# Performance work log

Measured on AMD Instinct MI355X. Metric: run time of the kernel, lower is better.

Reference implementation:

```python
import math
import jax, jax.numpy as jnp
import numpy as np

HIDDEN = 1024
HEADS = 16
HEAD_DIM = HIDDEN // HEADS
PRIME = 7
MAX_ITERS = 10
ENT_THRESH = 0.2
PRIME_SCALE = 1.0 / math.sqrt(PRIME * HEAD_DIM)
EPS = 1e-6


def setup_inputs() -> dict:
    key = jax.random.key(0)
    ks = jax.random.split(key, 6)
    B, S = 2, 2048
    w = 0.02
    return {
        "hidden_states": jax.random.normal(ks[0], (B, S, HIDDEN), jnp.float32),
        "q_w": jax.random.normal(ks[1], (HIDDEN, HIDDEN), jnp.float32) * w,
        "q_b": jnp.zeros((HIDDEN,), jnp.float32),
        "k_w": jax.random.normal(ks[2], (HIDDEN, HIDDEN), jnp.float32) * w,
        "k_b": jnp.zeros((HIDDEN,), jnp.float32),
        "v_w": jax.random.normal(ks[3], (HIDDEN, HIDDEN), jnp.float32) * w,
        "v_b": jnp.zeros((HIDDEN,), jnp.float32),
        "o_w": jax.random.normal(ks[4], (HIDDEN, HIDDEN), jnp.float32) * w,
        "o_b": jnp.zeros((HIDDEN,), jnp.float32),
        "attention_mask": jnp.ones((B, S), jnp.int32),
    }


def _split_heads(x):
    B, S, _ = x.shape
    return x.reshape(B, S, HEADS, HEAD_DIM).transpose(0, 2, 1, 3)


def reference(hidden_states, q_w, q_b, k_w, k_b, v_w, v_b, o_w, o_b, attention_mask):
    B, S, _ = hidden_states.shape
    # projections (torch Linear: x @ W^T + b)
    q = _split_heads(hidden_states @ q_w.T + q_b) * PRIME_SCALE  # [B,H,S,hd]
    k = _split_heads(hidden_states @ k_w.T + k_b)
    v = _split_heads(hidden_states @ v_w.T + v_b)

    scores = jnp.einsum("bhqd,bhkd->bhqk", q, k)  # [B,H,S,S]
    mask = attention_mask[:, None, None, :]
    scores = jnp.where(mask == 0, -jnp.inf, scores)
    attn = jax.nn.softmax(scores, axis=-1)  # dropout p=0 (eval)

    base = jnp.einsum("bhqk,bhkd->bhqd", attn, v)  # attention_weights @ v

    # entropy of the (fixed) attention weights: [B,H]
    entropy = -jnp.sum(attn * jnp.log(attn + EPS), axis=-1).mean(axis=-1)
    avg_entropy = entropy.mean()

    # loop never changes attn, so entropy is constant: either break at i=1 or run all
    full = base
    for i in range(1, MAX_ITERS):
        blend = 1.0 / (1.0 + math.exp(-i / MAX_ITERS))          # sigmoid(i/max)
        res_scale = 0.5 + 0.5 * blend                            # resonance scale
        full = (1.0 - blend) * full + blend * (res_scale * base)

    out_heads = jnp.where(avg_entropy < ENT_THRESH, base, full)  # [B,H,S,hd]

    merged = out_heads.transpose(0, 2, 1, 3).reshape(B, S, HIDDEN)
    return merged @ o_w.T + o_b
```

## Files before the change

### kernel.cpp

```cpp
#include <hip/hip_runtime.h>
#include <hip/hip_bf16.h>
#include <stdint.h>


#define PRIME_SCALE 0.047245559126654356f
#define LOG2E       1.4426950408889634f
#define LN2         0.6931471805599453f
#define QSCALE      (PRIME_SCALE * LOG2E)
#define BLEND_C     0.85096556f

#if __has_builtin(__builtin_amdgcn_exp2f)
#define EXP2(x) __builtin_amdgcn_exp2f(x)
#else
#define EXP2(x) exp2f(x)
#endif

typedef __attribute__((ext_vector_type(8))) short short8;
typedef __attribute__((ext_vector_type(4))) float f32x4;

__device__ __forceinline__ unsigned short f2bf(float x) {
    union { float f; unsigned int u; } v; v.f = x;
    unsigned int r = (v.u + 0x7fffu + ((v.u >> 16) & 1u)) >> 16;
    return (unsigned short)r;
}
__device__ __forceinline__ unsigned short f2bf_fast(float x) {
    union { float f; unsigned int u; } v; v.f = x;
    return (unsigned short)((v.u + 0x8000u) >> 16);
}
__device__ __forceinline__ float bf2f(unsigned short x) {
    union { unsigned int u; float f; } v; v.u = ((unsigned int)x) << 16;
    return v.f;
}
__device__ __forceinline__ unsigned cvtpk_bf16(float lo, float hi) {
    unsigned r;
    asm("v_cvt_pk_bf16_f32 %0, %1, %2" : "=v"(r) : "v"(lo), "v"(hi));
    return r;
}

__device__ __forceinline__ void glds16(const unsigned short* g, unsigned short* l) {
    __builtin_amdgcn_global_load_lds((const __attribute__((address_space(1))) unsigned int*)g,
                                     (__attribute__((address_space(3))) unsigned int*)l,
                                     16, 0, 0);
}

__global__ void zero_out_f32(float* p, int n) {
    int i = blockIdx.x * 256 + threadIdx.x;
    if (i < n) p[i] = 0.f;
}

__global__ __launch_bounds__(256) void cvt5(
    const float* __restrict__ s0, const float* __restrict__ s1, const float* __restrict__ s2,
    const float* __restrict__ s3, const float* __restrict__ s4,
    unsigned short* __restrict__ d0, unsigned short* __restrict__ d1, unsigned short* __restrict__ d2,
    unsigned short* __restrict__ d3, unsigned short* __restrict__ d4, float* entp)
{
    if (blockIdx.x == 0 && threadIdx.x == 0) entp[0] = 0.f;
    unsigned int i = blockIdx.x * 256 + threadIdx.x;
    const float* s; unsigned short* d; unsigned int off;
    if (i < (1u << 20)) { s = s0; d = d0; off = i; }
    else {
        unsigned int j = i - (1u << 20);
        unsigned int sel = j >> 18; off = j & 0x3FFFFu;
        s = sel == 0 ? s1 : sel == 1 ? s2 : sel == 2 ? s3 : s4;
        d = sel == 0 ? d1 : sel == 1 ? d2 : sel == 2 ? d3 : d4;
    }
    float4 v = ((const float4*)s)[off];
    ushort4 p; p.x = f2bf(v.x); p.y = f2bf(v.y); p.z = f2bf(v.z); p.w = f2bf(v.w);
    ((ushort4*)d)[off] = p;
}

__global__ __launch_bounds__(256) void gemm_qkv(
    const unsigned short* __restrict__ hsb,
    const unsigned short* __restrict__ qwb, const unsigned short* __restrict__ kwb,
    const unsigned short* __restrict__ vwb,
    const float* __restrict__ qb, const float* __restrict__ kb, const float* __restrict__ vb,
    unsigned short* __restrict__ Qo, unsigned short* __restrict__ Ko, unsigned short* __restrict__ Vto)
{
    const int bid = blockIdx.x;
    const int op = bid >> 8, local = bid & 255;
    const unsigned short *A, *B; const float* bias; unsigned short* C;
    int m0, n0, ldc, biasRow; float scale;
    if (op == 0)      { A = hsb; B = qwb; bias = qb; C = Qo;  m0 = (local >> 3) * 128; n0 = (local & 7) * 128;  ldc = 1024; biasRow = 0; scale = QSCALE; }
    else if (op == 1) { A = hsb; B = kwb; bias = kb; C = Ko;  m0 = (local >> 3) * 128; n0 = (local & 7) * 128;  ldc = 1024; biasRow = 0; scale = 1.f; }
    else              { A = vwb; B = hsb; bias = vb; C = Vto; m0 = (local >> 5) * 128; n0 = (local & 31) * 128; ldc = 4096; biasRow = 1; scale = 1.f; }

    __shared__ unsigned short As[128 * 32];
    __shared__ unsigned short Bs[128 * 32];
    const int t = threadIdx.x, lane = t & 63, w = t >> 6;
    const int quad = lane >> 4, l15 = lane & 15;
    const int wr = (w >> 1) * 64, wc = (w & 1) * 64;
    const int srow = lane >> 2, scol = (lane & 3) * 8;

    f32x4 acc[4][4];
#pragma unroll
    for (int i = 0; i < 4; ++i)
#pragma unroll
        for (int j = 0; j < 4; ++j) acc[i][j] = (f32x4){0.f, 0.f, 0.f, 0.f};

    for (int kk = 0; kk < 32; ++kk) {
        const int k0 = kk * 32;
#pragma unroll
        for (int j = 0; j < 2; ++j) {
            int row = (w * 2 + j) * 16 + srow;
            glds16(&A[(size_t)(m0 + row) * 1024 + k0 + scol], &As[(w * 2 + j) * 512]);
            glds16(&B[(size_t)(n0 + row) * 1024 + k0 + scol], &Bs[(w * 2 + j) * 512]);
        }
        __syncthreads();
        short8 af[4], bf[4];
#pragma unroll
        for (int mt = 0; mt < 4; ++mt) af[mt] = *(const short8*)&As[(wr + mt * 16 + l15) * 32 + quad * 8];
#pragma unroll
        for (int nt = 0; nt < 4; ++nt) bf[nt] = *(const short8*)&Bs[(wc + nt * 16 + l15) * 32 + quad * 8];
#pragma unroll
        for (int mt = 0; mt < 4; ++mt)
#pragma unroll
            for (int nt = 0; nt < 4; ++nt)
                acc[mt][nt] = __builtin_amdgcn_mfma_f32_16x16x32_bf16(af[mt], bf[nt], acc[mt][nt], 0, 0, 0);
        __syncthreads();
    }
#pragma unroll
    for (int mt = 0; mt < 4; ++mt) {
#pragma unroll
        for (int nt = 0; nt < 4; ++nt) {
            int n = n0 + wc + nt * 16 + l15;
#pragma unroll
            for (int r = 0; r < 4; ++r) {
                int m = m0 + wr + mt * 16 + quad * 4 + r;
                float bval = biasRow ? bias[m] : bias[n];
                C[(size_t)m * ldc + n] = f2bf((acc[mt][nt][r] + bval) * scale);
            }
        }
    }
}


#define QK_SOFTMAX(MASKED)                                                          \
    _Pragma("unroll")                                                               \
    for (int nt = 0; nt < 4; ++nt) {                                                \
        int krow = nt * 16 + l15;                                                   \
        short8 kf0 = *(const short8*)&Ks[cur][krow * 64 + ((quad ^ (krow & 7)) * 8)];       \
        short8 kf1 = *(const short8*)&Ks[cur][krow * 64 + (((quad + 4) ^ (krow & 7)) * 8)]; \
        f32x4 sv[4];                                                                \
        __builtin_amdgcn_s_setprio(1);                                              \
        _Pragma("unroll")                                                           \
        for (int st = 0; st < 4; ++st) {                                            \
            sv[st] = __builtin_amdgcn_mfma_f32_16x16x32_bf16(kf0, qa[st][0], (f32x4){0.f, 0.f, 0.f, 0.f}, 0, 0, 0); \
            sv[st] = __builtin_amdgcn_mfma_f32_16x16x32_bf16(kf1, qa[st][1], sv[st], 0, 0, 0); \
        }                                                                           \
        __builtin_amdgcn_s_setprio(0);                                              \
        unsigned mb = 0xFu;                                                         \
        if (MASKED) {                                                               \
            unsigned mw = (nt & 2) ? mwB : mwA;                                     \
            mb = (mw >> (((nt & 1) << 4) + (quad << 2))) & 0xFu;                    \
        }                                                                           \
        _Pragma("unroll")                                                           \
        for (int st = 0; st < 4; ++st) {                                            \
            float s0 = sv[st][0], s1 = sv[st][1], s2 = sv[st][2], s3 = sv[st][3];   \
            if (MASKED) {                                                           \
                s0 = (mb & 1u) ? s0 : -1.0e30f;                                     \
                s1 = (mb & 2u) ? s1 : -1.0e30f;                                     \
                s2 = (mb & 4u) ? s2 : -1.0e30f;                                     \
                s3 = (mb & 8u) ? s3 : -1.0e30f;                                     \
            }                                                                       \
            float p0 = EXP2(s0), p1 = EXP2(s1), p2 = EXP2(s2), p3 = EXP2(s3);       \
            l_r[st] += (p0 + p1) + (p2 + p3);                                       \
            T_r[st] += (p0 * s0 + p1 * s1) + (p2 * s2 + p3 * s3);                   \
            pk[nt][st][0] = cvtpk_bf16(p0, p1);                                     \
            pk[nt][st][1] = cvtpk_bf16(p2, p3);                                     \
        }                                                                           \
    }

__global__ __launch_bounds__(256, 2) void flash_split(
    const unsigned short* __restrict__ Q,
    const unsigned short* __restrict__ K,
    const unsigned short* __restrict__ Vt,
    const int* __restrict__ mask,
    unsigned short* __restrict__ O0, unsigned short* __restrict__ O1,
    float* __restrict__ lpart, float* __restrict__ Tpart)
{
    const int qt = blockIdx.x;
    const int bh = blockIdx.y;
    const int z  = blockIdx.z;
    const int b = bh >> 4, h = bh & 15;
    const int t = threadIdx.x, lane = t & 63, w = t >> 6;
    const int quad = lane >> 4, l15 = lane & 15;
    const int r8 = lane >> 3, ch8 = lane & 7;
    const int kt0 = z * 16, kt1 = kt0 + 16;
    unsigned short* __restrict__ Opart = z ? O1 : O0;

    __shared__ unsigned short Qs[256 * 64];
    __shared__ unsigned short Ks[2][64 * 64];
    __shared__ unsigned short Vs[2][64 * 64];

    const int* maskb = mask + b * 2048;

    {
        const int row0 = w * 16;
#pragma unroll
        for (int i = 0; i < 2; ++i) {
            int row = row0 + i * 8 + r8;
            int c = ch8 ^ (row & 7);
            glds16(&K[(size_t)(b * 2048 + kt0 * 64 + row) * 1024 + h * 64 + c * 8], &Ks[0][(row0 + i * 8) * 64]);
            glds16(&Vt[(size_t)(h * 64 + row) * 4096 + b * 2048 + kt0 * 64 + c * 8], &Vs[0][(row0 + i * 8) * 64]);
        }
    }
#pragma unroll
    for (int i = 0; i < 8; ++i) {
        int f = i * 256 + t; int row = f >> 3, c = f & 7;
        uint4 v = *(const uint4*)&Q[(size_t)(b * 2048 + qt * 256 + row) * 1024 + h * 64 + c * 8];
        int rx = row & 15;
        uint2 plo; plo.x = v.x; plo.y = v.y;
        uint2 phi; phi.x = v.z; phi.y = v.w;
        *(uint2*)&Qs[row * 64 + (((2 * c) ^ rx) << 2)]     = plo;
        *(uint2*)&Qs[row * 64 + (((2 * c + 1) ^ rx) << 2)] = phi;
    }
    __syncthreads();

    short8 qa[4][2];
#pragma unroll
    for (int st = 0; st < 4; ++st) {
        int prow = (w * 64 + st * 16 + l15) * 64;
#pragma unroll
        for (int hf = 0; hf < 2; ++hf) {
            int p0 = hf * 8 + quad * 2;
            union { uint2 u2[2]; short8 s8; } uu;
            uu.u2[0] = *(const uint2*)&Qs[prow + ((p0 ^ l15) << 2)];
            uu.u2[1] = *(const uint2*)&Qs[prow + (((p0 + 1) ^ l15) << 2)];
            qa[st][hf] = uu.s8;
        }
    }

    float l_r[4] = {0.f, 0.f, 0.f, 0.f}, T_r[4] = {0.f, 0.f, 0.f, 0.f};
    f32x4 o_acc[4][4];
#pragma unroll
    for (int st = 0; st < 4; ++st)
#pragma unroll
        for (int nt = 0; nt < 4; ++nt) o_acc[st][nt] = (f32x4){0.f, 0.f, 0.f, 0.f};

    int mv = maskb[kt0 * 64 + lane];

    for (int kt = kt0; kt < kt1; ++kt) {
        const int cur = kt & 1;
        int mv_next = 0;
        if (kt < kt1 - 1) {
            const int kn = (kt + 1) * 64;
            const int row0 = w * 16;
#pragma unroll
            for (int i = 0; i < 2; ++i) {
                int row = row0 + i * 8 + r8;
                int c = ch8 ^ (row & 7);
                glds16(&K[(size_t)(b * 2048 + kn + row) * 1024 + h * 64 + c * 8], &Ks[cur ^ 1][(row0 + i * 8) * 64]);
                glds16(&Vt[(size_t)(h * 64 + row) * 4096 + b * 2048 + kn + c * 8], &Vs[cur ^ 1][(row0 + i * 8) * 64]);
            }
            mv_next = maskb[kn + lane];
        }
        unsigned long long bal = __ballot(mv != 0);
        unsigned mwA = (unsigned)bal, mwB = (unsigned)(bal >> 32);

        unsigned pk[4][4][2];
        if ((mwA & mwB) == 0xFFFFFFFFu) {
            QK_SOFTMAX(0)
        } else {
            QK_SOFTMAX(1)
        }

#pragma unroll
        for (int ks = 0; ks < 2; ++ks) {
            short8 pa[4];
#pragma unroll
            for (int st = 0; st < 4; ++st) {
                unsigned a0 = pk[2 * ks][st][0], a1 = pk[2 * ks][st][1];
                unsigned b0 = pk[2 * ks + 1][st][0], b1 = pk[2 * ks + 1][st][1];
                asm("v_permlane32_swap_b32 %0, %1" : "+v"(a0), "+v"(b0));
                asm("v_permlane32_swap_b32 %0, %1" : "+v"(a1), "+v"(b1));
                asm("v_permlane16_swap_b32 %0, %1" : "+v"(a0), "+v"(b0));
                asm("v_permlane16_swap_b32 %0, %1" : "+v"(a1), "+v"(b1));
                union { unsigned u[4]; short8 s8; } uu;
                uu.u[0] = a0; uu.u[1] = a1; uu.u[2] = b0; uu.u[3] = b1;
                pa[st] = uu.s8;
            }
            __builtin_amdgcn_s_setprio(1);
#pragma unroll
            for (int nt = 0; nt < 4; ++nt) {
                int vrow = nt * 16 + l15;
                short8 vf = *(const short8*)&Vs[cur][vrow * 64 + ((((ks * 4 + quad)) ^ (vrow & 7)) * 8)];
#pragma unroll
                for (int st = 0; st < 4; ++st)
                    o_acc[st][nt] = __builtin_amdgcn_mfma_f32_16x16x32_bf16(pa[st], vf, o_acc[st][nt], 0, 0, 0);
            }
            __builtin_amdgcn_s_setprio(0);
        }
        __syncthreads();
        mv = mv_next;
    }

#pragma unroll
    for (int st = 0; st < 4; ++st) {
        float l = l_r[st], T = T_r[st];
        l += __shfl_xor(l, 16); T += __shfl_xor(T, 16);
        l += __shfl_xor(l, 32); T += __shfl_xor(T, 32);
        if (lane < 16) {
            int qrow = qt * 256 + w * 64 + st * 16 + l15;
            int li = z * 65536 + bh * 2048 + qrow;
            lpart[li] = l; Tpart[li] = T;
        }
#pragma unroll
        for (int r = 0; r < 4; ++r) {
            int mrow = b * 2048 + qt * 256 + w * 64 + st * 16 + quad * 4 + r;
#pragma unroll
            for (int nt = 0; nt < 4; ++nt)
                Opart[(size_t)mrow * 1024 + h * 64 + nt * 16 + l15] = f2bf_fast(o_acc[st][nt][r]);
        }
    }
}

__global__ __launch_bounds__(256) void combine_split(
    unsigned short* __restrict__ O0, const unsigned short* __restrict__ O1,
    const float* __restrict__ lpart)
{
    unsigned idx = blockIdx.x * 256 + threadIdx.x;
    int mrow = idx >> 8;
    int c4 = (idx & 255) << 2;
    int h = c4 >> 6;
    int b = mrow >> 11, qrow = mrow & 2047;
    int li = (b * 16 + h) * 2048 + qrow;
    float l = lpart[li] + lpart[65536 + li];
    float inv = 1.0f / l;

    ushort4 a = ((const ushort4*)O0)[idx];
    ushort4 c = ((const ushort4*)O1)[idx];
    ushort4 o;
    o.x = f2bf_fast((bf2f(a.x) + bf2f(c.x)) * inv);
    o.y = f2bf_fast((bf2f(a.y) + bf2f(c.y)) * inv);
    o.z = f2bf_fast((bf2f(a.z) + bf2f(c.z)) * inv);
    o.w = f2bf_fast((bf2f(a.w) + bf2f(c.w)) * inv);
    ((ushort4*)O0)[idx] = o;
}

__global__ __launch_bounds__(256) void entropy_k(
    const float* __restrict__ lpart, const float* __restrict__ Tpart,
    float* __restrict__ entp)
{
    __shared__ float wsum[4];
    int idx = blockIdx.x * 256 + threadIdx.x;
    float acc = 0.f;
#pragma unroll
    for (int i = 0; i < 4; ++i) {
        int r = idx * 4 + i;
        float l = lpart[r] + lpart[65536 + r];
        float T = Tpart[r] + Tpart[65536 + r];
        acc += __log2f(l) - T / l;
    }
    acc += __shfl_xor(acc, 1);
    acc += __shfl_xor(acc, 2);
    acc += __shfl_xor(acc, 4);
    acc += __shfl_xor(acc, 8);
    acc += __shfl_xor(acc, 16);
    acc += __shfl_xor(acc, 32);
    int lane = threadIdx.x & 63, w = threadIdx.x >> 6;
    if (lane == 0) wsum[w] = acc;
    __syncthreads();
    if (threadIdx.x == 0)
        atomicAdd(entp, LN2 * (wsum[0] + wsum[1] + wsum[2] + wsum[3]));
}

__global__ __launch_bounds__(256) void gemm_out_bf(
    const unsigned short* __restrict__ A, const unsigned short* __restrict__ Bw,
    const float* __restrict__ bias, const float* __restrict__ entp,
    float* __restrict__ C)
{
    const float avg = entp[0] * (1.0f / 65536.0f);
    const float scale = (avg < 0.2f) ? 1.0f : BLEND_C;

    const int m0 = blockIdx.x * 128;
    const int n0 = blockIdx.y * 64;
    __shared__ unsigned short As[128 * 32];
    __shared__ unsigned short Bs[64 * 32];
    const int t = threadIdx.x, lane = t & 63, w = t >> 6;
    const int quad = lane >> 4, l15 = lane & 15;
    const int wr = (w >> 1) * 64, wc = (w & 1) * 32;
    const int srow = lane >> 2, scol = (lane & 3) * 8;

    f32x4 acc[4][2];
#pragma unroll
    for (int i = 0; i < 4; ++i)
#pragma unroll
        for (int j = 0; j < 2; ++j) acc[i][j] = (f32x4){0.f, 0.f, 0.f, 0.f};

    for (int kk = 0; kk < 32; ++kk) {
        const int k0 = kk * 32;
#pragma unroll
        for (int j = 0; j < 2; ++j) {
            int row = (w * 2 + j) * 16 + srow;
            glds16(&A[(size_t)(m0 + row) * 1024 + k0 + scol], &As[(w * 2 + j) * 512]);
        }
        {
            int row = w * 16 + srow;
            glds16(&Bw[(size_t)(n0 + row) * 1024 + k0 + scol], &Bs[w * 512]);
        }
        __syncthreads();
        short8 af[4], bf[2];
#pragma unroll
        for (int mt = 0; mt < 4; ++mt) af[mt] = *(const short8*)&As[(wr + mt * 16 + l15) * 32 + quad * 8];
#pragma unroll
        for (int nt = 0; nt < 2; ++nt) bf[nt] = *(const short8*)&Bs[(wc + nt * 16 + l15) * 32 + quad * 8];
#pragma unroll
        for (int mt = 0; mt < 4; ++mt)
#pragma unroll
            for (int nt = 0; nt < 2; ++nt)
                acc[mt][nt] = __builtin_amdgcn_mfma_f32_16x16x32_bf16(af[mt], bf[nt], acc[mt][nt], 0, 0, 0);
        __syncthreads();
    }
#pragma unroll
    for (int mt = 0; mt < 4; ++mt) {
#pragma unroll
        for (int nt = 0; nt < 2; ++nt) {
            int n = n0 + wc + nt * 16 + l15;
#pragma unroll
            for (int r = 0; r < 4; ++r) {
                int m = m0 + wr + mt * 16 + quad * 4 + r;
                C[(size_t)m * 1024 + n] = scale * acc[mt][nt][r] + bias[n];
            }
        }
    }
}

extern "C" void kernel_launch(void* const* d_in, const int* in_sizes, int n_in,
                              void* d_out, int out_size, void* d_ws, size_t ws_size,
                              hipStream_t stream)
{
    const float* hs = (const float*)d_in[0];
    const float* qw = (const float*)d_in[1];
    const float* qb = (const float*)d_in[2];
    const float* kw = (const float*)d_in[3];
    const float* kb = (const float*)d_in[4];
    const float* vw = (const float*)d_in[5];
    const float* vb = (const float*)d_in[6];
    const float* ow = (const float*)d_in[7];
    const float* ob = (const float*)d_in[8];
    const int*   mask = (const int*)d_in[9];
    float* out = (float*)d_out;

    const size_t MB = 1024 * 1024;
    char* ws = (char*)d_ws;
    dim3 blk(256);

    if (ws_size >= 50 * MB) {
        unsigned short* hsb = (unsigned short*)(ws);
        unsigned short* Q   = (unsigned short*)(ws + 8 * MB);
        unsigned short* Kp  = (unsigned short*)(ws + 16 * MB);
        unsigned short* Vt  = (unsigned short*)(ws + 24 * MB);
        unsigned short* qwb = (unsigned short*)(ws + 32 * MB);
        unsigned short* kwb = (unsigned short*)(ws + 34 * MB);
        unsigned short* vwb = (unsigned short*)(ws + 36 * MB);
        unsigned short* owb = (unsigned short*)(ws + 38 * MB);
        float* entp         = (float*)(ws + 40 * MB);
        unsigned short* Op1 = (unsigned short*)(ws + 41 * MB);
        float* lpart        = (float*)(ws + 49 * MB);
        float* Tpart        = (float*)(ws + 49 * MB + 524288);
        unsigned short* Op0 = hsb;

        cvt5<<<dim3(8192), blk, 0, stream>>>(hs, qw, kw, vw, ow, hsb, qwb, kwb, vwb, owb, entp);
        gemm_qkv<<<dim3(768), blk, 0, stream>>>(hsb, qwb, kwb, vwb, qb, kb, vb, Q, Kp, Vt);
        flash_split<<<dim3(8, 32, 2), blk, 0, stream>>>(Q, Kp, Vt, mask, Op0, Op1, lpart, Tpart);
        combine_split<<<dim3(4096), blk, 0, stream>>>(Op0, Op1, lpart);
        entropy_k<<<dim3(64), blk, 0, stream>>>(lpart, Tpart, entp);
        gemm_out_bf<<<dim3(32, 16), blk, 0, stream>>>(Op0, owb, ob, entp, out);
    } else {
        zero_out_f32<<<dim3((out_size + 255) / 256), blk, 0, stream>>>(out, out_size);
    }
}
```

Measured before the change: 205.1 us.

## Split each flash K tile across two warp groups with in-LDS output reduction

The flash attention kernel now runs 512 threads per block. Two groups of four warps each process half of every 64-key tile, and their partial O accumulators and l/T sums are reduced through shared memory at the end. Q fragments are loaded straight from global memory into registers, which removes the Q staging buffer in LDS and cuts shared memory per block so more blocks can be resident. The cost is a cross-warp reduction epilogue with extra barriers, plus duplicated Q loads and K/V tile traffic shared by more waves.

```diff
diff --git a/kernel.cpp b/kernel.cpp
--- a/kernel.cpp
+++ b/kernel.cpp
@@ -136,10 +136,10 @@
 
 #define QK_SOFTMAX(MASKED)                                                          \
     _Pragma("unroll")                                                               \
-    for (int nt = 0; nt < 4; ++nt) {                                                \
-        int krow = nt * 16 + l15;                                                   \
-        short8 kf0 = *(const short8*)&Ks[cur][krow * 64 + ((quad ^ (krow & 7)) * 8)];       \
-        short8 kf1 = *(const short8*)&Ks[cur][krow * 64 + (((quad + 4) ^ (krow & 7)) * 8)]; \
+    for (int nt2 = 0; nt2 < 2; ++nt2) {                                             \
+        int krow = wk * 32 + nt2 * 16 + l15;                                        \
+        short8 kf0 = *(const short8*)&Ks[cur * 4096 + krow * 64 + ((quad ^ (krow & 7)) * 8)];       \
+        short8 kf1 = *(const short8*)&Ks[cur * 4096 + krow * 64 + (((quad + 4) ^ (krow & 7)) * 8)]; \
         f32x4 sv[4];                                                                \
         __builtin_amdgcn_s_setprio(1);                                              \
         _Pragma("unroll")                                                           \
@@ -149,10 +149,7 @@
         }                                                                           \
         __builtin_amdgcn_s_setprio(0);                                              \
         unsigned mb = 0xFu;                                                         \
-        if (MASKED) {                                                               \
-            unsigned mw = (nt & 2) ? mwB : mwA;                                     \
-            mb = (mw >> (((nt & 1) << 4) + (quad << 2))) & 0xFu;                    \
-        }                                                                           \
+        if (MASKED) mb = (mw >> ((nt2 << 4) + (quad << 2))) & 0xFu;                 \
         _Pragma("unroll")                                                           \
         for (int st = 0; st < 4; ++st) {                                            \
             float s0 = sv[st][0], s1 = sv[st][1], s2 = sv[st][2], s3 = sv[st][3];   \
@@ -165,12 +162,12 @@
             float p0 = EXP2(s0), p1 = EXP2(s1), p2 = EXP2(s2), p3 = EXP2(s3);       \
             l_r[st] += (p0 + p1) + (p2 + p3);                                       \
             T_r[st] += (p0 * s0 + p1 * s1) + (p2 * s2 + p3 * s3);                   \
-            pk[nt][st][0] = cvtpk_bf16(p0, p1);                                     \
-            pk[nt][st][1] = cvtpk_bf16(p2, p3);                                     \
+            pk[nt2][st][0] = cvtpk_bf16(p0, p1);                                    \
+            pk[nt2][st][1] = cvtpk_bf16(p2, p3);                                    \
         }                                                                           \
     }
 
-__global__ __launch_bounds__(256, 2) void flash_split(
+__global__ __launch_bounds__(512, 4) void flash_split(
     const unsigned short* __restrict__ Q,
     const unsigned short* __restrict__ K,
     const unsigned short* __restrict__ Vt,
@@ -183,51 +180,33 @@
     const int z  = blockIdx.z;
     const int b = bh >> 4, h = bh & 15;
     const int t = threadIdx.x, lane = t & 63, w = t >> 6;
+    const int wq = w & 3, wk = w >> 2;
     const int quad = lane >> 4, l15 = lane & 15;
     const int r8 = lane >> 3, ch8 = lane & 7;
     const int kt0 = z * 16, kt1 = kt0 + 16;
     unsigned short* __restrict__ Opart = z ? O1 : O0;
 
-    __shared__ unsigned short Qs[256 * 64];
-    __shared__ unsigned short Ks[2][64 * 64];
-    __shared__ unsigned short Vs[2][64 * 64];
+    __shared__ __align__(16) unsigned short smem[16384];
+    unsigned short* Ks = smem;
+    unsigned short* Vs = smem + 8192;
 
     const int* maskb = mask + b * 2048;
 
     {
-        const int row0 = w * 16;
-#pragma unroll
-        for (int i = 0; i < 2; ++i) {
-            int row = row0 + i * 8 + r8;
-            int c = ch8 ^ (row & 7);
-            glds16(&K[(size_t)(b * 2048 + kt0 * 64 + row) * 1024 + h * 64 + c * 8], &Ks[0][(row0 + i * 8) * 64]);
-            glds16(&Vt[(size_t)(h * 64 + row) * 4096 + b * 2048 + kt0 * 64 + c * 8], &Vs[0][(row0 + i * 8) * 64]);
-        }
-    }
-#pragma unroll
-    for (int i = 0; i < 8; ++i) {
-        int f = i * 256 + t; int row = f >> 3, c = f & 7;
-        uint4 v = *(const uint4*)&Q[(size_t)(b * 2048 + qt * 256 + row) * 1024 + h * 64 + c * 8];
-        int rx = row & 15;
-        uint2 plo; plo.x = v.x; plo.y = v.y;
-        uint2 phi; phi.x = v.z; phi.y = v.w;
-        *(uint2*)&Qs[row * 64 + (((2 * c) ^ rx) << 2)]     = plo;
-        *(uint2*)&Qs[row * 64 + (((2 * c + 1) ^ rx) << 2)] = phi;
-    }
-    __syncthreads();
+        int row = w * 8 + r8;
+        int c = ch8 ^ (row & 7);
+        glds16(&K[(size_t)(b * 2048 + kt0 * 64 + row) * 1024 + h * 64 + c * 8], &Ks[(w * 8) * 64]);
+        glds16(&Vt[(size_t)(h * 64 + row) * 4096 + b * 2048 + kt0 * 64 + c * 8], &Vs[(w * 8) * 64]);
+    }
 
     short8 qa[4][2];
 #pragma unroll
     for (int st = 0; st < 4; ++st) {
-        int prow = (w * 64 + st * 16 + l15) * 64;
-#pragma unroll
-        for (int hf = 0; hf < 2; ++hf) {
-            int p0 = hf * 8 + quad * 2;
-            union { uint2 u2[2]; short8 s8; } uu;
-            uu.u2[0] = *(const uint2*)&Qs[prow + ((p0 ^ l15) << 2)];
-            uu.u2[1] = *(const uint2*)&Qs[prow + (((p0 + 1) ^ l15) << 2)];
-            qa[st][hf] = uu.s8;
-        }
+        size_t qrow = (size_t)(b * 2048 + qt * 256 + wq * 64 + st * 16 + l15) * 1024 + h * 64;
+        union { uint4 v; short8 s8; } u0, u1;
+        u0.v = *(const uint4*)&Q[qrow + quad * 8];
+        u1.v = *(const uint4*)&Q[qrow + 32 + quad * 8];
+        qa[st][0] = u0.s8; qa[st][1] = u1.s8;
     }
 
     float l_r[4] = {0.f, 0.f, 0.f, 0.f}, T_r[4] = {0.f, 0.f, 0.f, 0.f};
@@ -238,61 +217,59 @@
         for (int nt = 0; nt < 4; ++nt) o_acc[st][nt] = (f32x4){0.f, 0.f, 0.f, 0.f};
 
     int mv = maskb[kt0 * 64 + lane];
+    __syncthreads();
 
     for (int kt = kt0; kt < kt1; ++kt) {
         const int cur = kt & 1;
         int mv_next = 0;
         if (kt < kt1 - 1) {
             const int kn = (kt + 1) * 64;
-            const int row0 = w * 16;
-#pragma unroll
-            for (int i = 0; i < 2; ++i) {
-                int row = row0 + i * 8 + r8;
-                int c = ch8 ^ (row & 7);
-                glds16(&K[(size_t)(b * 2048 + kn + row) * 1024 + h * 64 + c * 8], &Ks[cur ^ 1][(row0 + i * 8) * 64]);
-                glds16(&Vt[(size_t)(h * 64 + row) * 4096 + b * 2048 + kn + c * 8], &Vs[cur ^ 1][(row0 + i * 8) * 64]);
-            }
+            int row = w * 8 + r8;
+            int c = ch8 ^ (row & 7);
+            glds16(&K[(size_t)(b * 2048 + kn + row) * 1024 + h * 64 + c * 8], &Ks[(cur ^ 1) * 4096 + (w * 8) * 64]);
+            glds16(&Vt[(size_t)(h * 64 + row) * 4096 + b * 2048 + kn + c * 8], &Vs[(cur ^ 1) * 4096 + (w * 8) * 64]);
             mv_next = maskb[kn + lane];
         }
         unsigned long long bal = __ballot(mv != 0);
-        unsigned mwA = (unsigned)bal, mwB = (unsigned)(bal >> 32);
-
-        unsigned pk[4][4][2];
-        if ((mwA & mwB) == 0xFFFFFFFFu) {
+        unsigned mw = wk ? (unsigned)(bal >> 32) : (unsigned)bal;
+
+        unsigned pk[2][4][2];
+        if (mw == 0xFFFFFFFFu) {
             QK_SOFTMAX(0)
         } else {
             QK_SOFTMAX(1)
         }
 
-#pragma unroll
-        for (int ks = 0; ks < 2; ++ks) {
-            short8 pa[4];
-#pragma unroll
-            for (int st = 0; st < 4; ++st) {
-                unsigned a0 = pk[2 * ks][st][0], a1 = pk[2 * ks][st][1];
-                unsigned b0 = pk[2 * ks + 1][st][0], b1 = pk[2 * ks + 1][st][1];
-                asm("v_permlane32_swap_b32 %0, %1" : "+v"(a0), "+v"(b0));
-                asm("v_permlane32_swap_b32 %0, %1" : "+v"(a1), "+v"(b1));
-                asm("v_permlane16_swap_b32 %0, %1" : "+v"(a0), "+v"(b0));
-                asm("v_permlane16_swap_b32 %0, %1" : "+v"(a1), "+v"(b1));
-                union { unsigned u[4]; short8 s8; } uu;
-                uu.u[0] = a0; uu.u[1] = a1; uu.u[2] = b0; uu.u[3] = b1;
-                pa[st] = uu.s8;
-            }
-            __builtin_amdgcn_s_setprio(1);
-#pragma unroll
-            for (int nt = 0; nt < 4; ++nt) {
-                int vrow = nt * 16 + l15;
-                short8 vf = *(const short8*)&Vs[cur][vrow * 64 + ((((ks * 4 + quad)) ^ (vrow & 7)) * 8)];
-#pragma unroll
-                for (int st = 0; st < 4; ++st)
-                    o_acc[st][nt] = __builtin_amdgcn_mfma_f32_16x16x32_bf16(pa[st], vf, o_acc[st][nt], 0, 0, 0);
-            }
-            __builtin_amdgcn_s_setprio(0);
-        }
+        short8 pa[4];
+#pragma unroll
+        for (int st = 0; st < 4; ++st) {
+            unsigned a0 = pk[0][st][0], a1 = pk[0][st][1];
+            unsigned b0 = pk[1][st][0], b1 = pk[1][st][1];
+            asm("v_permlane32_swap_b32 %0, %1" : "+v"(a0), "+v"(b0));
+            asm("v_permlane32_swap_b32 %0, %1" : "+v"(a1), "+v"(b1));
+            asm("v_permlane16_swap_b32 %0, %1" : "+v"(a0), "+v"(b0));
+            asm("v_permlane16_swap_b32 %0, %1" : "+v"(a1), "+v"(b1));
+            union { unsigned u[4]; short8 s8; } uu;
+            uu.u[0] = a0; uu.u[1] = a1; uu.u[2] = b0; uu.u[3] = b1;
+            pa[st] = uu.s8;
+        }
+        __builtin_amdgcn_s_setprio(1);
+#pragma unroll
+        for (int nt = 0; nt < 4; ++nt) {
+            int vrow = nt * 16 + l15;
+            short8 vf = *(const short8*)&Vs[cur * 4096 + vrow * 64 + (((wk * 4 + quad) ^ (vrow & 7)) * 8)];
+#pragma unroll
+            for (int st = 0; st < 4; ++st)
+                o_acc[st][nt] = __builtin_amdgcn_mfma_f32_16x16x32_bf16(pa[st], vf, o_acc[st][nt], 0, 0, 0);
+        }
+        __builtin_amdgcn_s_setprio(0);
         __syncthreads();
         mv = mv_next;
     }
+
+    float* lsum = (float*)Vs;
+    float* Tsum = (float*)Vs + 512;
+    f32x4* osum = (f32x4*)Ks;
 
 #pragma unroll
     for (int st = 0; st < 4; ++st) {
@@ -300,17 +277,44 @@
         l += __shfl_xor(l, 16); T += __shfl_xor(T, 16);
         l += __shfl_xor(l, 32); T += __shfl_xor(T, 32);
         if (lane < 16) {
-            int qrow = qt * 256 + w * 64 + st * 16 + l15;
-            int li = z * 65536 + bh * 2048 + qrow;
-            lpart[li] = l; Tpart[li] = T;
-        }
-#pragma unroll
-        for (int r = 0; r < 4; ++r) {
-            int mrow = b * 2048 + qt * 256 + w * 64 + st * 16 + quad * 4 + r;
+            int li = ((wk * 4 + wq) * 4 + st) * 16 + l15;
+            lsum[li] = l; Tsum[li] = T;
+        }
+    }
+
+#pragma unroll
+    for (int st = 0; st < 4; ++st) {
+        if (wk == 1) {
 #pragma unroll
             for (int nt = 0; nt < 4; ++nt)
-                Opart[(size_t)mrow * 1024 + h * 64 + nt * 16 + l15] = f2bf_fast(o_acc[st][nt][r]);
-        }
+                osum[(wq * 4 + nt) * 64 + lane] = o_acc[st][nt];
+        }
+        __syncthreads();
+        if (wk == 0) {
+            if (st == 0 && lane < 16) {
+#pragma unroll
+                for (int s2 = 0; s2 < 4; ++s2) {
+                    int i0 = ((0 * 4 + wq) * 4 + s2) * 16 + l15;
+                    int i1 = ((1 * 4 + wq) * 4 + s2) * 16 + l15;
+                    int qrow = qt * 256 + wq * 64 + s2 * 16 + l15;
+                    int li = z * 65536 + bh * 2048 + qrow;
+                    lpart[li] = lsum[i0] + lsum[i1];
+                    Tpart[li] = Tsum[i0] + Tsum[i1];
+                }
+            }
+            f32x4 osr[4];
+#pragma unroll
+            for (int nt = 0; nt < 4; ++nt)
+                osr[nt] = o_acc[st][nt] + osum[(wq * 4 + nt) * 64 + lane];
+#pragma unroll
+            for (int r = 0; r < 4; ++r) {
+                int mrow = b * 2048 + qt * 256 + wq * 64 + st * 16 + quad * 4 + r;
+#pragma unroll
+                for (int nt = 0; nt < 4; ++nt)
+                    Opart[(size_t)mrow * 1024 + h * 64 + nt * 16 + l15] = f2bf_fast(osr[nt][r]);
+            }
+        }
+        __syncthreads();
     }
 }
 
@@ -462,7 +466,7 @@
 
         cvt5<<<dim3(8192), blk, 0, stream>>>(hs, qw, kw, vw, ow, hsb, qwb, kwb, vwb, owb, entp);
         gemm_qkv<<<dim3(768), blk, 0, stream>>>(hsb, qwb, kwb, vwb, qb, kb, vb, Q, Kp, Vt);
-        flash_split<<<dim3(8, 32, 2), blk, 0, stream>>>(Q, Kp, Vt, mask, Op0, Op1, lpart, Tpart);
+        flash_split<<<dim3(8, 32, 2), dim3(512), 0, stream>>>(Q, Kp, Vt, mask, Op0, Op1, lpart, Tpart);
         combine_split<<<dim3(4096), blk, 0, stream>>>(Op0, Op1, lpart);
         entropy_k<<<dim3(64), blk, 0, stream>>>(lpart, Tpart, entp);
         gemm_out_bf<<<dim3(32, 16), blk, 0, stream>>>(Op0, owb, ob, entp, out);
```

Measured after the change: 554.2 us. 2.7x slower.

## Load Q directly to registers, precompute mask bits, deepen K/V prefetch to two tiles

Applied to the files above, without the earlier changes.

Q fragments are now read straight from global memory into MFMA registers, which removes the 32KB Qs shared buffer and its staging pass. The mask is packed once into a shared bitmask, replacing a per-iteration global load plus ballot. K/V loads are issued two tiles ahead with explicit vmcnt waits and raw barriers, so global loads overlap more compute. The smaller LDS footprint may also allow more resident blocks, but the hand-written waitcnt/barrier sequence is fragile.

```diff
diff --git a/kernel.cpp b/kernel.cpp
--- a/kernel.cpp
+++ b/kernel.cpp
@@ -133,6 +133,19 @@
     }
 }
 
+
+#define STAGE(KT, BUF) do {                                                         \
+    int kn_ = (KT) * 64;                                                            \
+    _Pragma("unroll")                                                               \
+    for (int i_ = 0; i_ < 2; ++i_) {                                                \
+        int row_ = w * 16 + i_ * 8 + r8;                                            \
+        int c_ = ch8 ^ (row_ & 7);                                                  \
+        glds16(&K[(size_t)(b * 2048 + kn_ + row_) * 1024 + h * 64 + c_ * 8],        \
+               &Ks[BUF][(w * 16 + i_ * 8) * 64]);                                   \
+        glds16(&Vt[(size_t)(h * 64 + row_) * 4096 + b * 2048 + kn_ + c_ * 8],       \
+               &Vs[BUF][(w * 16 + i_ * 8) * 64]);                                   \
+    }                                                                               \
+} while (0)
 
 #define QK_SOFTMAX(MASKED)                                                          \
     _Pragma("unroll")                                                               \
@@ -188,47 +201,32 @@
     const int kt0 = z * 16, kt1 = kt0 + 16;
     unsigned short* __restrict__ Opart = z ? O1 : O0;
 
-    __shared__ unsigned short Qs[256 * 64];
-    __shared__ unsigned short Ks[2][64 * 64];
-    __shared__ unsigned short Vs[2][64 * 64];
-
-    const int* maskb = mask + b * 2048;
+    __shared__ __align__(16) unsigned short Ks[2][64 * 64];
+    __shared__ __align__(16) unsigned short Vs[2][64 * 64];
+    __shared__ unsigned int maskBits[64];
+
+    short8 qa[4][2];
+#pragma unroll
+    for (int st = 0; st < 4; ++st) {
+        size_t qrow = (size_t)(b * 2048 + qt * 256 + w * 64 + st * 16 + l15) * 1024 + h * 64;
+        union { uint4 v; short8 s8; } u0, u1;
+        u0.v = *(const uint4*)&Q[qrow + quad * 8];
+        u1.v = *(const uint4*)&Q[qrow + 32 + quad * 8];
+        qa[st][0] = u0.s8; qa[st][1] = u1.s8;
+    }
 
     {
-        const int row0 = w * 16;
-#pragma unroll
-        for (int i = 0; i < 2; ++i) {
-            int row = row0 + i * 8 + r8;
-            int c = ch8 ^ (row & 7);
-            glds16(&K[(size_t)(b * 2048 + kt0 * 64 + row) * 1024 + h * 64 + c * 8], &Ks[0][(row0 + i * 8) * 64]);
-            glds16(&Vt[(size_t)(h * 64 + row) * 4096 + b * 2048 + kt0 * 64 + c * 8], &Vs[0][(row0 + i * 8) * 64]);
-        }
-    }
-#pragma unroll
-    for (int i = 0; i < 8; ++i) {
-        int f = i * 256 + t; int row = f >> 3, c = f & 7;
-        uint4 v = *(const uint4*)&Q[(size_t)(b * 2048 + qt * 256 + row) * 1024 + h * 64 + c * 8];
-        int rx = row & 15;
-        uint2 plo; plo.x = v.x; plo.y = v.y;
-        uint2 phi; phi.x = v.z; phi.y = v.w;
-        *(uint2*)&Qs[row * 64 + (((2 * c) ^ rx) << 2)]     = plo;
-        *(uint2*)&Qs[row * 64 + (((2 * c + 1) ^ rx) << 2)] = phi;
-    }
-    __syncthreads();
-
-    short8 qa[4][2];
-#pragma unroll
-    for (int st = 0; st < 4; ++st) {
-        int prow = (w * 64 + st * 16 + l15) * 64;
-#pragma unroll
-        for (int hf = 0; hf < 2; ++hf) {
-            int p0 = hf * 8 + quad * 2;
-            union { uint2 u2[2]; short8 s8; } uu;
-            uu.u2[0] = *(const uint2*)&Qs[prow + ((p0 ^ l15) << 2)];
-            uu.u2[1] = *(const uint2*)&Qs[prow + (((p0 + 1) ^ l15) << 2)];
-            qa[st][hf] = uu.s8;
-        }
-    }
+        const int4* mp = (const int4*)(mask + b * 2048 + t * 8);
+        int4 a = mp[0], c = mp[1];
+        unsigned bits = (unsigned)(a.x != 0)       | ((unsigned)(a.y != 0) << 1)
+                      | ((unsigned)(a.z != 0) << 2) | ((unsigned)(a.w != 0) << 3)
+                      | ((unsigned)(c.x != 0) << 4) | ((unsigned)(c.y != 0) << 5)
+                      | ((unsigned)(c.z != 0) << 6) | ((unsigned)(c.w != 0) << 7);
+        ((unsigned char*)maskBits)[t] = (unsigned char)bits;
+    }
+
+    STAGE(kt0, 0);
+    STAGE(kt0 + 1, 1);
 
     float l_r[4] = {0.f, 0.f, 0.f, 0.f}, T_r[4] = {0.f, 0.f, 0.f, 0.f};
     f32x4 o_acc[4][4];
@@ -237,25 +235,13 @@
 #pragma unroll
         for (int nt = 0; nt < 4; ++nt) o_acc[st][nt] = (f32x4){0.f, 0.f, 0.f, 0.f};
 
-    int mv = maskb[kt0 * 64 + lane];
+    asm volatile("s_waitcnt lgkmcnt(0)" ::: "memory");
+    asm volatile("s_waitcnt vmcnt(4)" ::: "memory");
+    asm volatile("s_barrier" ::: "memory");
 
     for (int kt = kt0; kt < kt1; ++kt) {
         const int cur = kt & 1;
-        int mv_next = 0;
-        if (kt < kt1 - 1) {
-            const int kn = (kt + 1) * 64;
-            const int row0 = w * 16;
-#pragma unroll
-            for (int i = 0; i < 2; ++i) {
-                int row = row0 + i * 8 + r8;
-                int c = ch8 ^ (row & 7);
-                glds16(&K[(size_t)(b * 2048 + kn + row) * 1024 + h * 64 + c * 8], &Ks[cur ^ 1][(row0 + i * 8) * 64]);
-                glds16(&Vt[(size_t)(h * 64 + row) * 4096 + b * 2048 + kn + c * 8], &Vs[cur ^ 1][(row0 + i * 8) * 64]);
-            }
-            mv_next = maskb[kn + lane];
-        }
-        unsigned long long bal = __ballot(mv != 0);
-        unsigned mwA = (unsigned)bal, mwB = (unsigned)(bal >> 32);
+        unsigned mwA = maskBits[kt * 2], mwB = maskBits[kt * 2 + 1];
 
         unsigned pk[4][4][2];
         if ((mwA & mwB) == 0xFFFFFFFFu) {
@@ -290,8 +276,17 @@
             }
             __builtin_amdgcn_s_setprio(0);
         }
-        __syncthreads();
-        mv = mv_next;
+
+        if (kt < kt1 - 1) {
+            asm volatile("s_barrier" ::: "memory");
+            if (kt < kt1 - 2) {
+                STAGE(kt + 2, cur);
+                asm volatile("s_waitcnt vmcnt(4)" ::: "memory");
+            } else {
+                asm volatile("s_waitcnt vmcnt(0)" ::: "memory");
+            }
+            asm volatile("s_barrier" ::: "memory");
+        }
     }
 
 #pragma unroll
```

New measurement: 204.5 us. Within noise of the previous version (-0.3%).
